# Kernel tuning notes

Measured on AMD Instinct MI355X. Metric: run time of the kernel, lower is better.

Reference implementation:

```python
import jax, jax.numpy as jnp
import numpy as np

D_MODEL = 1024
N_HEADS = 16
HEAD_DIM = D_MODEL // N_HEADS  # 64


def setup_inputs() -> dict:
    key = jax.random.key(0)
    k1, k2, k3 = jax.random.split(key, 3)
    x = jax.random.normal(k1, (2, 2048, D_MODEL), dtype=jnp.float32)
    # nn.Linear(d, 3d, bias=False): store transposed so y = x @ W
    w_qkv = jax.random.normal(k2, (D_MODEL, 3 * D_MODEL), dtype=jnp.float32) * (D_MODEL ** -0.5)
    w_proj = jax.random.normal(k3, (D_MODEL, D_MODEL), dtype=jnp.float32) * (D_MODEL ** -0.5)
    return {"x": x, "w_qkv": w_qkv, "w_proj": w_proj}


def reference(x, w_qkv, w_proj):
    b, n, _ = x.shape
    qkv = x @ w_qkv  # [b, n, 3*d_model]
    # einops 'b n (h d qkv) -> qkv b h n d': qkv axis is innermost of the split
    qkv = qkv.reshape(b, n, N_HEADS, HEAD_DIM, 3)
    q = jnp.moveaxis(qkv[..., 0], 1, 2)  # [b, h, n, d]
    k = jnp.moveaxis(qkv[..., 1], 1, 2)
    v = jnp.moveaxis(qkv[..., 2], 1, 2)
    scale = HEAD_DIM ** -0.5
    scores = jnp.einsum('bhqd,bhkd->bhqk', q, k) * scale  # [b, h, n, n]
    causal = jnp.tril(jnp.ones((n, n), dtype=bool))
    scores = jnp.where(causal[None, None], scores, -jnp.inf)
    attn = jax.nn.softmax(scores, axis=-1)
    out = jnp.einsum('bhqk,bhkd->bhqd', attn, v)  # [b, h, n, d]
    out = jnp.moveaxis(out, 1, 2).reshape(b, n, D_MODEL)  # 'b h n d -> b n (h d)'
    return out @ w_proj
```

## Files before the change

### kernel.cpp

```cpp
#include <hip/hip_runtime.h>
#include <cstdint>
#include <cstddef>

#define D_MODEL 1024
#define N_HEADS 16
#define HEAD_DIM 64
#define SEQ 2048
#define BATCH 2

typedef __attribute__((ext_vector_type(8))) short bf16x8;
typedef __attribute__((ext_vector_type(4))) float f32x4;

__device__ __forceinline__ unsigned cvtpk_bf16(float lo, float hi) {
    unsigned r;
    asm("v_cvt_pk_bf16_f32 %0, %1, %2" : "=v"(r) : "v"(lo), "v"(hi));
    return r;
}
__device__ __forceinline__ unsigned short f2bf_hw(float f) {
    return (unsigned short)cvtpk_bf16(f, 0.f);
}

__device__ __forceinline__ void gload_lds16(const unsigned short* g, unsigned short* l) {
    __builtin_amdgcn_global_load_lds(
        (const __attribute__((address_space(1))) unsigned int*)g,
        (__attribute__((address_space(3))) unsigned int*)l, 16, 0, 0);
}

#define WAITCNT_VM4 0x0F74
#define WAITCNT_VM0 0x0F70

__global__ __launch_bounds__(256) void fused_convert_kernel(
    const float* __restrict__ X, unsigned short* __restrict__ Xb,
    const float* __restrict__ Wq, unsigned short* __restrict__ Wqt,
    const float* __restrict__ Wp, unsigned short* __restrict__ Wpt)
{
    const int blk = blockIdx.x;
    const int tid = threadIdx.x;
    __shared__ float t[32][33];

    if (blk < 2048) {
        const int idx = blk * 256 + tid;
        const float4* src = (const float4*)X;
        float4 v0 = src[idx * 2], v1 = src[idx * 2 + 1];
        uint4 o;
        o.x = cvtpk_bf16(v0.x, v0.y);
        o.y = cvtpk_bf16(v0.z, v0.w);
        o.z = cvtpk_bf16(v1.x, v1.y);
        o.w = cvtpk_bf16(v1.z, v1.w);
        ((uint4*)Xb)[idx] = o;
    } else if (blk < 5120) {
        const int bb = blk - 2048;
        const int c0 = (bb % 96) * 32, r0 = (bb / 96) * 32;
        const int a = tid & 31, b = tid >> 5;
#pragma unroll
        for (int i = 0; i < 32; i += 8)
            t[b + i][a] = Wq[(size_t)(r0 + b + i) * (3 * D_MODEL) + c0 + a];
        __syncthreads();
#pragma unroll
        for (int i = 0; i < 32; i += 8) {
            const int c = c0 + b + i;
            const int which = c % 3;
            const int np = which * 1024 + c / 3;
            const float s = (which == 0) ? 0.125f : 1.0f;
            Wqt[(size_t)np * D_MODEL + r0 + a] = f2bf_hw(t[a][b + i] * s);
        }
    } else {
        const int bb = blk - 5120;
        const int c0 = (bb % 32) * 32, r0 = (bb / 32) * 32;
        const int a = tid & 31, b = tid >> 5;
#pragma unroll
        for (int i = 0; i < 32; i += 8)
            t[b + i][a] = Wp[(size_t)(r0 + b + i) * D_MODEL + c0 + a];
        __syncthreads();
#pragma unroll
        for (int i = 0; i < 32; i += 8)
            Wpt[(size_t)(c0 + b + i) * D_MODEL + r0 + a] = f2bf_hw(t[a][b + i]);
    }
}

#define GEMM_PIPE3_BODY(A_, B_, KBASE, NITER, BX_, BY_)                        \
    const int tid = threadIdx.x;                                               \
    const int w = tid >> 6, lane = tid & 63;                                   \
    const int l15 = lane & 15, quad = lane >> 4;                               \
    const int wr = w >> 1, wc = w & 1;                                         \
    const int row0 = (BY_) * 128, col0 = (BX_) * 128;                          \
    __shared__ unsigned short As[3][4096];                                     \
    __shared__ unsigned short Bs[3][4096];                                     \
    const f32x4 zero4 = {0.f, 0.f, 0.f, 0.f};                                  \
    f32x4 acc[4][4];                                                           \
    _Pragma("unroll") for (int i = 0; i < 4; i++)                              \
        _Pragma("unroll") for (int j = 0; j < 4; j++) acc[i][j] = zero4;       \
    auto stage_ = [&](int sb_, int kt_) {                                      \
        const int k0 = (KBASE) + kt_ * 32 + quad * 8;                          \
        _Pragma("unroll") for (int i = 0; i < 2; i++) {                        \
            const int f = w * 2 + i;                                           \
            gload_lds16((A_) + (size_t)(row0 + f * 16 + l15) * D_MODEL + k0,   \
                        &As[sb_][f * 512 + lane * 8]);                         \
            gload_lds16((B_) + (size_t)(col0 + f * 16 + l15) * D_MODEL + k0,   \
                        &Bs[sb_][f * 512 + lane * 8]);                         \
        }                                                                      \
    };                                                                         \
    stage_(0, 0);                                                              \
    stage_(1, 1);                                                              \
    int sb = 0;                                                                \
    for (int kt = 0; kt < (NITER); kt++) {                                     \
        if (kt < (NITER) - 1) {                                                \
            __builtin_amdgcn_s_waitcnt(WAITCNT_VM4);                           \
            __builtin_amdgcn_s_barrier();                                      \
            if (kt + 2 < (NITER)) stage_((sb + 2 > 2) ? sb - 1 : sb + 2, kt + 2); \
        } else {                                                               \
            __builtin_amdgcn_s_waitcnt(WAITCNT_VM0);                           \
            __builtin_amdgcn_s_barrier();                                      \
        }                                                                      \
        bf16x8 af[4], bfr[4];                                                  \
        _Pragma("unroll") for (int i = 0; i < 4; i++)                          \
            af[i] = *(const bf16x8*)&As[sb][(wr * 4 + i) * 512 + lane * 8];    \
        _Pragma("unroll") for (int j = 0; j < 4; j++)                          \
            bfr[j] = *(const bf16x8*)&Bs[sb][(wc * 4 + j) * 512 + lane * 8];   \
        __builtin_amdgcn_s_setprio(1);                                         \
        _Pragma("unroll") for (int i = 0; i < 4; i++)                          \
            _Pragma("unroll") for (int j = 0; j < 4; j++)                      \
                acc[i][j] = __builtin_amdgcn_mfma_f32_16x16x32_bf16(           \
                    af[i], bfr[j], acc[i][j], 0, 0, 0);                        \
        __builtin_amdgcn_s_setprio(0);                                         \
        sb = (sb == 2) ? 0 : sb + 1;                                           \
    }

__global__ __launch_bounds__(256) void gemm_qkv_mfma(
    const unsigned short* __restrict__ A, const unsigned short* __restrict__ B,
    unsigned short* __restrict__ Q, unsigned short* __restrict__ Kq,
    unsigned short* __restrict__ Vt)
{
    const int lin = blockIdx.x + 24 * blockIdx.y;
    const int xcd = lin & 7, t = lin >> 3;
    const int bx = (xcd & 1) * 12 + t % 12;
    const int by = (xcd >> 1) * 8 + t / 12;
    GEMM_PIPE3_BODY(A, B, 0, 32, bx, by)
    const int nbase = col0 + wc * 64;
    const int which = col0 >> 10;
    if (which < 2) {
        unsigned short* const dst = (which == 0) ? Q : Kq;
#pragma unroll
        for (int i = 0; i < 4; i++) {
            const int rowb = row0 + wr * 64 + i * 16 + quad * 4;
            const int bb = rowb >> 11, n = rowb & (SEQ - 1);
#pragma unroll
            for (int rp = 0; rp < 2; rp++) {
#pragma unroll
                for (int j = 0; j < 4; j++) {
                    const unsigned u = cvtpk_bf16(acc[i][j][2 * rp], acc[i][j][2 * rp + 1]);
                    const int idx = (nbase + j * 16 + l15) & 1023;
                    const int h = idx >> 6, dd = idx & 63;
                    unsigned short* p =
                        dst + (((size_t)(bb * N_HEADS + h)) * SEQ + n + 2 * rp) * HEAD_DIM + dd;
                    p[0] = (unsigned short)u;
                    p[HEAD_DIM] = (unsigned short)(u >> 16);
                }
            }
        }
    } else {
        unsigned short* vt = &As[0][0];
        const int n0 = row0 & (SEQ - 1);
        const int bb = row0 >> 11;
        const int vbase = col0 & 1023;
        __syncthreads();
#pragma unroll
        for (int half = 0; half < 2; half++) {
            if (wc == half) {
#pragma unroll
                for (int i = 0; i < 4; i++) {
                    const int nl = wr * 64 + i * 16 + quad * 4;
#pragma unroll
                    for (int rp = 0; rp < 2; rp++) {
#pragma unroll
                        for (int j = 0; j < 4; j++) {
                            const unsigned u =
                                cvtpk_bf16(acc[i][j][2 * rp], acc[i][j][2 * rp + 1]);
                            const int c_loc = j * 16 + l15;
                            *(unsigned*)&vt[c_loc * 136 + nl + 2 * rp] = u;
                        }
                    }
                }
            }
            __syncthreads();
#pragma unroll
            for (int pass = 0; pass < 4; pass++) {
                const int c_loc = pass * 16 + (tid >> 4);
                const int t16 = tid & 15;
                const uint4 v = *(const uint4*)&vt[c_loc * 136 + t16 * 8];
                const int vc = vbase + half * 64 + c_loc;
                *(uint4*)&Vt[((size_t)(bb * N_HEADS + (vc >> 6)) * HEAD_DIM
                              + (vc & 63)) * SEQ + n0 + t16 * 8] = v;
            }
            if (half == 0) __syncthreads();
        }
    }
}

__global__ __launch_bounds__(256) void gemm_proj_splitk(
    const unsigned short* __restrict__ A, const unsigned short* __restrict__ B,
    float* __restrict__ Outp)
{
    const int lin = blockIdx.x + 8 * blockIdx.y;
    const int xcd = lin & 7, t = lin >> 3;
    const int bx = (xcd & 1) * 4 + t % 4;
    const int by = (xcd >> 1) * 8 + t / 4;
    const int kbase = blockIdx.z * 512;
    GEMM_PIPE3_BODY(A, B, kbase, 16, bx, by)
#pragma unroll
    for (int i = 0; i < 4; i++) {
#pragma unroll
        for (int r = 0; r < 4; r++) {
            const int row = row0 + wr * 64 + i * 16 + quad * 4 + r;
#pragma unroll
            for (int j = 0; j < 4; j++) {
                const int c = col0 + wc * 64 + j * 16 + l15;
                atomicAdd(&Outp[(size_t)row * D_MODEL + c], acc[i][j][r]);
            }
        }
    }
}

__global__ __launch_bounds__(256) void flash_attn_kernel(
    const unsigned short* __restrict__ Q,
    const unsigned short* __restrict__ K,
    const unsigned short* __restrict__ Vt,
    unsigned short* __restrict__ O)
{
    const int idx = blockIdx.x;
    const int bh = idx & 31;
    const int qt2 = idx >> 5;
    const int hi = qt2 >> 3, lo = qt2 & 7;
    const int qt = (hi == 0) ? lo : (hi == 1) ? 31 - lo : (hi == 2) ? lo + 8 : 23 - lo;

    const int tid = threadIdx.x;
    const int w = tid >> 6, lane = tid & 63;
    const int l15 = lane & 15, quad = lane >> 4;

    __shared__ unsigned short Ks[2][4096];
    __shared__ unsigned short Vs[2][4096];
    __shared__ unsigned short Ps[4][1024];

    bf16x8 qf[2];
    {
        const unsigned short* qrow =
            Q + ((size_t)bh * SEQ + qt * 64 + w * 16 + l15) * HEAD_DIM;
        qf[0] = *(const bf16x8*)(qrow + quad * 8);
        qf[1] = *(const bf16x8*)(qrow + 32 + quad * 8);
    }

    const f32x4 zero4 = {0.f, 0.f, 0.f, 0.f};
    f32x4 o_acc[4] = {zero4, zero4, zero4, zero4};
    float m_i = -1e30f, l_i = 0.f;

    auto stage = [&](int bf, int kt_t) {
        const int key0 = kt_t * 64;
#pragma unroll
        for (int i = 0; i < 2; i++) {
            const int f = w * 2 + i;
            const int ct = f >> 1, kh = f & 1;
            gload_lds16(K + ((size_t)bh * SEQ + key0 + ct * 16 + l15) * HEAD_DIM
                          + kh * 32 + quad * 8,
                        &Ks[bf][f * 512 + lane * 8]);
            gload_lds16(Vt + ((size_t)bh * HEAD_DIM + ct * 16 + l15) * SEQ
                           + key0 + kh * 32 + quad * 8,
                        &Vs[bf][f * 512 + lane * 8]);
        }
    };

    stage(0, 0);
    int buf = 0;

    const int qg = qt * 64 + w * 16 + l15;

    for (int kt = 0; kt <= qt; kt++) {
        __syncthreads();
        if (kt < qt) stage(buf ^ 1, kt + 1);

        f32x4 st[4] = {zero4, zero4, zero4, zero4};
        __builtin_amdgcn_s_setprio(1);
#pragma unroll
        for (int kh = 0; kh < 2; kh++) {
#pragma unroll
            for (int ct = 0; ct < 4; ct++) {
                bf16x8 kf = *(const bf16x8*)&Ks[buf][(ct * 2 + kh) * 512 + lane * 8];
                st[ct] = __builtin_amdgcn_mfma_f32_16x16x32_bf16(kf, qf[kh], st[ct], 0, 0, 0);
            }
        }
        __builtin_amdgcn_s_setprio(0);

        float mt = -1e30f;
        if (kt == qt) {
#pragma unroll
            for (int ct = 0; ct < 4; ct++) {
#pragma unroll
                for (int r = 0; r < 4; r++) {
                    const int kg = kt * 64 + ct * 16 + quad * 4 + r;
                    float v = (kg > qg) ? -1e30f : st[ct][r];
                    st[ct][r] = v;
                    mt = fmaxf(mt, v);
                }
            }
        } else {
#pragma unroll
            for (int ct = 0; ct < 4; ct++)
#pragma unroll
                for (int r = 0; r < 4; r++)
                    mt = fmaxf(mt, st[ct][r]);
        }
        mt = fmaxf(mt, __shfl_xor(mt, 16));
        mt = fmaxf(mt, __shfl_xor(mt, 32));

        float mn = m_i;
        if (!__all(mt <= m_i + 8.0f)) {
            mn = fmaxf(m_i, mt);
            const float alpha = __expf(m_i - mn);
            m_i = mn;
            l_i *= alpha;
            float ar[4];
#pragma unroll
            for (int r = 0; r < 4; r++)
                ar[r] = __shfl(alpha, (lane & 48) | (quad * 4 + r));
#pragma unroll
            for (int dt = 0; dt < 4; dt++)
#pragma unroll
                for (int r = 0; r < 4; r++)
                    o_acc[dt][r] *= ar[r];
        }

        float ls = 0.f;
#pragma unroll
        for (int ct = 0; ct < 4; ct++) {
            const float p0 = __expf(st[ct][0] - mn);
            const float p1 = __expf(st[ct][1] - mn);
            const float p2 = __expf(st[ct][2] - mn);
            const float p3 = __expf(st[ct][3] - mn);
            ls += (p0 + p1) + (p2 + p3);
            uint2 pk2;
            pk2.x = cvtpk_bf16(p0, p1);
            pk2.y = cvtpk_bf16(p2, p3);
            const int addr = (ct >> 1) * 512 + ((ct & 1) * 2 + (quad >> 1)) * 128
                           + l15 * 8 + (quad & 1) * 4;
            *(uint2*)&Ps[w][addr] = pk2;
        }
        l_i += ls;

        __builtin_amdgcn_s_setprio(1);
#pragma unroll
        for (int kh = 0; kh < 2; kh++) {
            bf16x8 pa = *(const bf16x8*)&Ps[w][kh * 512 + quad * 128 + l15 * 8];
#pragma unroll
            for (int dt = 0; dt < 4; dt++) {
                bf16x8 vf = *(const bf16x8*)&Vs[buf][(dt * 2 + kh) * 512 + lane * 8];
                o_acc[dt] = __builtin_amdgcn_mfma_f32_16x16x32_bf16(pa, vf, o_acc[dt], 0, 0, 0);
            }
        }
        __builtin_amdgcn_s_setprio(0);
        buf ^= 1;
    }

    l_i += __shfl_xor(l_i, 16);
    l_i += __shfl_xor(l_i, 32);
    const float linv = 1.0f / l_i;
    float lr[4];
#pragma unroll
    for (int r = 0; r < 4; r++)
        lr[r] = __shfl(linv, (lane & 48) | (quad * 4 + r));

    const int b = bh >> 4, h = bh & 15;
#pragma unroll
    for (int r = 0; r < 4; r++) {
        const int q = qt * 64 + w * 16 + quad * 4 + r;
        unsigned short* orow = O + ((size_t)b * SEQ + q) * D_MODEL + h * HEAD_DIM;
#pragma unroll
        for (int dt = 0; dt < 4; dt++)
            orow[dt * 16 + l15] = f2bf_hw(o_acc[dt][r] * lr[r]);
    }
}

extern "C" void kernel_launch(void* const* d_in, const int* in_sizes, int n_in,
                              void* d_out, int out_size, void* d_ws, size_t ws_size,
                              hipStream_t stream) {
    const float* x      = (const float*)d_in[0];
    const float* w_qkv  = (const float*)d_in[1];
    const float* w_proj = (const float*)d_in[2];
    float* out = (float*)d_out;

    unsigned short* Xb  = (unsigned short*)d_ws;
    unsigned short* Wqt = Xb  + (size_t)4 * 1024 * 1024;
    unsigned short* Wpt = Wqt + (size_t)3 * 1024 * 1024;
    unsigned short* Qb  = Wpt + (size_t)1 * 1024 * 1024;
    unsigned short* Kb  = Qb  + (size_t)4 * 1024 * 1024;
    unsigned short* Vb  = Kb  + (size_t)4 * 1024 * 1024;
    unsigned short* Vtb = Vb  + (size_t)4 * 1024 * 1024;
    unsigned short* Ob  = Vtb + (size_t)4 * 1024 * 1024;

    hipMemsetAsync(out, 0, (size_t)BATCH * SEQ * D_MODEL * sizeof(float), stream);

    fused_convert_kernel<<<dim3(6144), 256, 0, stream>>>(
        x, Xb, w_qkv, Wqt, w_proj, Wpt);

    gemm_qkv_mfma<<<dim3(3 * D_MODEL / 128, BATCH * SEQ / 128), 256, 0, stream>>>(
        Xb, Wqt, Qb, Kb, Vtb);

    flash_attn_kernel<<<dim3(SEQ / 64 * BATCH * N_HEADS), 256, 0, stream>>>(
        Qb, Kb, Vtb, Ob);

    gemm_proj_splitk<<<dim3(D_MODEL / 128, BATCH * SEQ / 128, 2), 256, 0, stream>>>(
        Ob, Wpt, out);
}
```

Before: 224.1 us.

## Replace split-K atomics in projection GEMM with intra-block K split and LDS reduction

The output projection GEMM no longer launches two K-halves as separate blocks that atomically add into a zeroed output. Each block now has 512 threads: two groups of four waves each take one K half and reduce their partial tiles through shared memory before a plain store. This removes the output memset and the float atomics. The cost is larger blocks with double-sized LDS staging buffers, which may reduce occupancy, plus extra barriers in the epilogue.

```diff
diff --git a/kernel.cpp b/kernel.cpp
--- a/kernel.cpp
+++ b/kernel.cpp
@@ -197,7 +197,7 @@
     }
 }
 
-__global__ __launch_bounds__(256) void gemm_proj_splitk(
+__global__ __launch_bounds__(512, 2) void gemm_proj_fused(
     const unsigned short* __restrict__ A, const unsigned short* __restrict__ B,
     float* __restrict__ Outp)
 {
@@ -205,19 +205,96 @@
     const int xcd = lin & 7, t = lin >> 3;
     const int bx = (xcd & 1) * 4 + t % 4;
     const int by = (xcd >> 1) * 8 + t / 4;
-    const int kbase = blockIdx.z * 512;
-    GEMM_PIPE3_BODY(A, B, kbase, 16, bx, by)
-#pragma unroll
-    for (int i = 0; i < 4; i++) {
-#pragma unroll
-        for (int r = 0; r < 4; r++) {
-            const int row = row0 + wr * 64 + i * 16 + quad * 4 + r;
-#pragma unroll
-            for (int j = 0; j < 4; j++) {
-                const int c = col0 + wc * 64 + j * 16 + l15;
-                atomicAdd(&Outp[(size_t)row * D_MODEL + c], acc[i][j][r]);
-            }
-        }
+
+    const int tid = threadIdx.x;
+    const int w = tid >> 6, lane = tid & 63;
+    const int half = w >> 2, wl = w & 3;
+    const int l15 = lane & 15, quad = lane >> 4;
+    const int wr = wl >> 1, wc = wl & 1;
+    const int row0 = by * 128, col0 = bx * 128;
+    const int kbase = half * 512;
+
+    __shared__ unsigned short As[2][3][4096];
+    __shared__ unsigned short Bs[2][3][4096];
+
+    const f32x4 zero4 = {0.f, 0.f, 0.f, 0.f};
+    f32x4 acc[4][4];
+#pragma unroll
+    for (int i = 0; i < 4; i++)
+#pragma unroll
+        for (int j = 0; j < 4; j++) acc[i][j] = zero4;
+
+    auto stage_ = [&](int sb_, int kt_) {
+        const int k0 = kbase + kt_ * 32 + quad * 8;
+#pragma unroll
+        for (int i = 0; i < 2; i++) {
+            const int f = wl * 2 + i;
+            gload_lds16(A + (size_t)(row0 + f * 16 + l15) * D_MODEL + k0,
+                        &As[half][sb_][f * 512 + lane * 8]);
+            gload_lds16(B + (size_t)(col0 + f * 16 + l15) * D_MODEL + k0,
+                        &Bs[half][sb_][f * 512 + lane * 8]);
+        }
+    };
+
+    stage_(0, 0);
+    stage_(1, 1);
+    int sb = 0;
+    for (int kt = 0; kt < 16; kt++) {
+        if (kt < 15) {
+            __builtin_amdgcn_s_waitcnt(WAITCNT_VM4);
+            __builtin_amdgcn_s_barrier();
+            if (kt + 2 < 16) stage_((sb + 2 > 2) ? sb - 1 : sb + 2, kt + 2);
+        } else {
+            __builtin_amdgcn_s_waitcnt(WAITCNT_VM0);
+            __builtin_amdgcn_s_barrier();
+        }
+        bf16x8 af[4], bfr[4];
+#pragma unroll
+        for (int i = 0; i < 4; i++)
+            af[i] = *(const bf16x8*)&As[half][sb][(wr * 4 + i) * 512 + lane * 8];
+#pragma unroll
+        for (int j = 0; j < 4; j++)
+            bfr[j] = *(const bf16x8*)&Bs[half][sb][(wc * 4 + j) * 512 + lane * 8];
+        __builtin_amdgcn_s_setprio(1);
+#pragma unroll
+        for (int i = 0; i < 4; i++)
+#pragma unroll
+            for (int j = 0; j < 4; j++)
+                acc[i][j] = __builtin_amdgcn_mfma_f32_16x16x32_bf16(
+                    af[i], bfr[j], acc[i][j], 0, 0, 0);
+        __builtin_amdgcn_s_setprio(0);
+        sb = (sb == 2) ? 0 : sb + 1;
+    }
+
+    __syncthreads();
+    float* rb = (float*)As;
+    const int rbase = (wl * 64 + lane) * 4;
+#pragma unroll
+    for (int p = 0; p < 2; p++) {
+        if (half == 1) {
+#pragma unroll
+            for (int ii = 0; ii < 2; ii++)
+#pragma unroll
+                for (int j = 0; j < 4; j++)
+                    *(f32x4*)&rb[(ii * 4 + j) * 1024 + rbase] = acc[p * 2 + ii][j];
+        }
+        __syncthreads();
+        if (half == 0) {
+#pragma unroll
+            for (int ii = 0; ii < 2; ii++) {
+                const int i = p * 2 + ii;
+                const int rowb = row0 + wr * 64 + i * 16 + quad * 4;
+#pragma unroll
+                for (int j = 0; j < 4; j++) {
+                    const f32x4 other = *(const f32x4*)&rb[(ii * 4 + j) * 1024 + rbase];
+                    const int c = col0 + wc * 64 + j * 16 + l15;
+#pragma unroll
+                    for (int r = 0; r < 4; r++)
+                        Outp[(size_t)(rowb + r) * D_MODEL + c] = acc[i][j][r] + other[r];
+                }
+            }
+        }
+        if (p == 0) __syncthreads();
     }
 }
 
@@ -395,8 +472,6 @@
     unsigned short* Vtb = Vb  + (size_t)4 * 1024 * 1024;
     unsigned short* Ob  = Vtb + (size_t)4 * 1024 * 1024;
 
-    hipMemsetAsync(out, 0, (size_t)BATCH * SEQ * D_MODEL * sizeof(float), stream);
-
     fused_convert_kernel<<<dim3(6144), 256, 0, stream>>>(
         x, Xb, w_qkv, Wqt, w_proj, Wpt);
 
@@ -406,6 +481,6 @@
     flash_attn_kernel<<<dim3(SEQ / 64 * BATCH * N_HEADS), 256, 0, stream>>>(
         Qb, Kb, Vtb, Ob);
 
-    gemm_proj_splitk<<<dim3(D_MODEL / 128, BATCH * SEQ / 128, 2), 256, 0, stream>>>(
+    gemm_proj_fused<<<dim3(D_MODEL / 128, BATCH * SEQ / 128), 512, 0, stream>>>(
         Ob, Wpt, out);
 }
```

Result: faster. 200.4 us (-10.6%).
